# Kernel tuning notes

Measured on AMD Instinct MI355X. Metric: run time of the kernel, lower is better.

The kernel has to match this reference:

```python
import jax, jax.numpy as jnp
import numpy as np

BATCH, SEQ, DIMS, HEADS = 4, 2048, 1024, 16
HEAD_DIM = DIMS // HEADS          # 64
ROT = HEAD_DIM // 2               # 32
BASE = 10000.0


def setup_inputs() -> dict:
    key = jax.random.key(0)
    k1, k2, k3, k4 = jax.random.split(key, 4)
    x = jax.random.normal(k1, (BATCH, SEQ, DIMS), jnp.float32)
    thetas = jax.random.normal(k2, (ROT,), jnp.float32) * 0.02
    theta_scale = jnp.ones((1,), jnp.float32)
    # nn.init.orthogonal_ equivalent
    a = jax.random.normal(k3, (HEAD_DIM, HEAD_DIM), jnp.float32)
    r_matrix, _ = jnp.linalg.qr(a)
    inv_freq = 1.0 / (BASE ** (jnp.arange(0, HEAD_DIM, 2, dtype=jnp.float32) / HEAD_DIM))
    # r_pairs: torch rand(rot,2)*head_dim then .long() -> ints in [0, head_dim)
    pairs = jax.random.randint(k4, (ROT, 2), 0, HEAD_DIM, dtype=jnp.int32)
    return {"x": x, "thetas": thetas, "theta_scale": theta_scale,
            "r_matrix": r_matrix, "inv_freq": inv_freq, "pairs": pairs}


def _forward(x, thetas, theta_scale, r_matrix, inv_freq, pairs):
    B, S, D = x.shape
    hd = r_matrix.shape[0]
    H = D // hd
    ts = theta_scale[0]
    xf = x.reshape(-1, hd)  # (B*S*H, hd)

    # Sequential Givens rotations: x @ G_k, applied as 2-column updates.
    # G[i,i]=c, G[j,j]=c, G[i,j]=-s, G[j,i]=s. If i==j, sequential torch
    def body(xx, k):
        i, j = pairs[k, 0], pairs[k, 1]
        th = thetas[k] * ts
        c, s = jnp.cos(th), jnp.sin(th)
        xi = xx[:, i]
        xj = xx[:, j]
        ni = xi * c + xj * s
        nj = jnp.where(i == j, xi * s, xj * c - xi * s)
        xx = xx.at[:, i].set(ni)
        xx = xx.at[:, j].set(nj)  # overwrites column i when i == j
        return xx, None

    xf, _ = jax.lax.scan(body, xf, jnp.arange(pairs.shape[0]))
    xf = xf @ r_matrix
    xh = xf.reshape(B, S, H, hd)

    # rotary sin/cos encoding (concatenated halves, not interleaved)
    pos = jnp.arange(S, dtype=x.dtype)[:, None]          # (S, 1)
    si = pos * inv_freq[None, :]                          # (S, hd//2)
    sin = jnp.sin(si)[None, :, None, :]                   # (1, S, 1, hd//2)
    cos = jnp.cos(si)[None, :, None, :]
    x1, x2 = xh[..., ::2], xh[..., 1::2]
    out = jnp.concatenate([x1 * cos - x2 * sin, x1 * sin + x2 * cos], axis=-1)
    return out.reshape(B, S, D) * jnp.sqrt(jnp.asarray(D, x.dtype))


def reference(x, thetas, theta_scale, r_matrix, inv_freq, pairs):
    return _forward(x, thetas, theta_scale, r_matrix, inv_freq, pairs)
```

## Files before the change

kernel.cpp:

```cpp
#include <hip/hip_runtime.h>
#include <math.h>

#define SEQ    2048
#define ROT    32
#define NTILES 2048

__global__ __launch_bounds__(256) void build_w_kernel(
    const float* __restrict__ thetas,
    const float* __restrict__ theta_scale,
    const float* __restrict__ R,
    const int*   __restrict__ pairs,
    float*       __restrict__ Wp)
{
    __shared__ float A[64 * 65];
    const int t = threadIdx.x;

    #pragma unroll
    for (int i = 0; i < 16; ++i) {
        int e = i * 256 + t;
        int r = e >> 6, c = e & 63;
        A[r * 65 + c] = (r == c) ? 1.0f : 0.0f;
    }
    __syncthreads();

    if (t < 64) {
        const float ts = theta_scale[0];
        float* Ar = &A[t * 65];
        for (int k = 0; k < ROT; ++k) {
            int i = pairs[2 * k], j = pairs[2 * k + 1];
            float th = thetas[k] * ts;
            float c = cosf(th), s = sinf(th);
            float ai = Ar[i], aj = Ar[j];
            if (i != j) { Ar[i] = c * ai + s * aj; Ar[j] = c * aj - s * ai; }
            else        { Ar[i] = s * ai; }
        }
    }
    __syncthreads();

    const int r = (blockIdx.x << 2) + (t >> 6);
    const int c = t & 63;
    const float* Ar = &A[r * 65];
    float acc = 0.0f;
    #pragma unroll 8
    for (int k = 0; k < 64; ++k)
        acc = fmaf(Ar[k], R[k * 64 + c], acc);
    const int dest = (c & 1) ? (32 + (c >> 1)) : (c >> 1);
    Wp[r * 64 + dest] = 32.0f * acc;
}

__global__ __launch_bounds__(256) void rotary_main_kernel(
    const float* __restrict__ x,
    const float* __restrict__ Wp,
    const float* __restrict__ inv_freq,
    float*       __restrict__ out)
{
    __shared__ float  Xs[64 * 65];
    __shared__ float  Ws[64 * 64];
    __shared__ float2 SC[4 * 32];

    const int T    = blockIdx.x;
    const int t    = threadIdx.x;
    const int lane = t & 63;

    const float4* xg = (const float4*)(x + (size_t)T * 4096);
    #pragma unroll
    for (int i = 0; i < 4; ++i) {
        int g = i * 256 + t;
        float4 v = xg[g];
        int row = g >> 4;
        int col = (g & 15) << 2;
        float* p = &Xs[row * 65 + col];
        p[0] = v.x; p[1] = v.y; p[2] = v.z; p[3] = v.w;
    }
    {
        const float4* wg  = (const float4*)Wp;
        float4*       ws4 = (float4*)Ws;
        #pragma unroll
        for (int i = 0; i < 4; ++i) {
            int g = i * 256 + t;
            ws4[g] = wg[g];
        }
    }
    if (t < 128) {
        int pp = t >> 5, d = t & 31;
        int pos = (T * 4 + pp) & (SEQ - 1);
        float ang = (float)pos * inv_freq[d];
        float sv, cv;
        sincosf(ang, &sv, &cv);
        SC[t] = make_float2(cv, sv);
    }
    __syncthreads();

    const int cq = __builtin_amdgcn_readfirstlane(t >> 6);
    const float* xr = &Xs[lane * 65];
    const float* wc = &Ws[cq * 16];

    float acc[16];
    #pragma unroll
    for (int m = 0; m < 16; ++m) acc[m] = 0.0f;

    #pragma unroll 8
    for (int k = 0; k < 64; ++k) {
        float xv = xr[k];
        const float4 w0 = *(const float4*)(wc + k * 64);
        const float4 w1 = *(const float4*)(wc + k * 64 + 4);
        const float4 w2 = *(const float4*)(wc + k * 64 + 8);
        const float4 w3 = *(const float4*)(wc + k * 64 + 12);
        acc[ 0] = fmaf(xv, w0.x, acc[ 0]);
        acc[ 1] = fmaf(xv, w0.y, acc[ 1]);
        acc[ 2] = fmaf(xv, w0.z, acc[ 2]);
        acc[ 3] = fmaf(xv, w0.w, acc[ 3]);
        acc[ 4] = fmaf(xv, w1.x, acc[ 4]);
        acc[ 5] = fmaf(xv, w1.y, acc[ 5]);
        acc[ 6] = fmaf(xv, w1.z, acc[ 6]);
        acc[ 7] = fmaf(xv, w1.w, acc[ 7]);
        acc[ 8] = fmaf(xv, w2.x, acc[ 8]);
        acc[ 9] = fmaf(xv, w2.y, acc[ 9]);
        acc[10] = fmaf(xv, w2.z, acc[10]);
        acc[11] = fmaf(xv, w2.w, acc[11]);
        acc[12] = fmaf(xv, w3.x, acc[12]);
        acc[13] = fmaf(xv, w3.y, acc[13]);
        acc[14] = fmaf(xv, w3.z, acc[14]);
        acc[15] = fmaf(xv, w3.w, acc[15]);
    }

    __syncthreads();
    #pragma unroll
    for (int m = 0; m < 16; ++m)
        Xs[lane * 65 + cq * 16 + m] = acc[m];
    __syncthreads();

    float* og = out + (size_t)T * 4096;
    const int w = t >> 6;
    #pragma unroll
    for (int u = 0; u < 16; ++u) {
        int row = u * 4 + w;
        int d   = lane & 31;
        float yd = Xs[row * 65 + d];
        float y2 = Xs[row * 65 + 32 + d];
        float2 cs = SC[(row >> 4) * 32 + d];
        float o = (lane < 32) ? (yd * cs.x - y2 * cs.y)
                              : (yd * cs.y + y2 * cs.x);
        og[u * 256 + t] = o;
    }
}

extern "C" void kernel_launch(void* const* d_in, const int* in_sizes, int n_in,
                              void* d_out, int out_size, void* d_ws, size_t ws_size,
                              hipStream_t stream) {
    const float* x           = (const float*)d_in[0];
    const float* thetas      = (const float*)d_in[1];
    const float* theta_scale = (const float*)d_in[2];
    const float* r_matrix    = (const float*)d_in[3];
    const float* inv_freq    = (const float*)d_in[4];
    const int*   pairs       = (const int*)d_in[5];
    float*       out         = (float*)d_out;
    float*       Wp          = (float*)d_ws;

    build_w_kernel<<<16, 256, 0, stream>>>(thetas, theta_scale, r_matrix, pairs, Wp);
    rotary_main_kernel<<<NTILES, 256, 0, stream>>>(x, Wp, inv_freq, out);
}
```

Measured before the change: 119.1 us.

## Use 4x8 register tiles with XOR-swizzled transposed X tile and direct epilogue

Each block now handles 128 rows instead of 64. Each thread computes a 4x8 output tile from a transposed, XOR-swizzled shared-memory copy of X, so both operands are read as float4 and each loaded value is reused more times. The W column permutation is dropped: the rotary epilogue pairs adjacent accumulator columns in registers and writes float4 results straight to global memory, which removes the second shared-memory round trip and its barriers. Shared memory per block grows, which may lower occupancy, and the transposing stores into shared memory are scalar and scattered.

```diff
diff --git a/kernel.cpp b/kernel.cpp
--- a/kernel.cpp
+++ b/kernel.cpp
@@ -3,14 +3,15 @@
 
 #define SEQ    2048
 #define ROT    32
-#define NTILES 2048
+#define ROWS_PER_BLOCK 128
+#define NTILES (131072 / ROWS_PER_BLOCK)
 
 __global__ __launch_bounds__(256) void build_w_kernel(
     const float* __restrict__ thetas,
     const float* __restrict__ theta_scale,
     const float* __restrict__ R,
     const int*   __restrict__ pairs,
-    float*       __restrict__ Wp)
+    float*       __restrict__ W)
 {
     __shared__ float A[64 * 65];
     const int t = threadIdx.x;
@@ -44,104 +45,97 @@
     #pragma unroll 8
     for (int k = 0; k < 64; ++k)
         acc = fmaf(Ar[k], R[k * 64 + c], acc);
-    const int dest = (c & 1) ? (32 + (c >> 1)) : (c >> 1);
-    Wp[r * 64 + dest] = 32.0f * acc;
+    W[r * 64 + c] = 32.0f * acc;
 }
 
 __global__ __launch_bounds__(256) void rotary_main_kernel(
     const float* __restrict__ x,
-    const float* __restrict__ Wp,
+    const float* __restrict__ W,
     const float* __restrict__ inv_freq,
     float*       __restrict__ out)
 {
-    __shared__ float  Xs[64 * 65];
-    __shared__ float  Ws[64 * 64];
-    __shared__ float2 SC[4 * 32];
+    __shared__ float Xt[64 * 128];
+    __shared__ float Ws[64 * 64];
+    __shared__ float SCc[8 * 32];
+    __shared__ float SCs[8 * 32];
 
-    const int T    = blockIdx.x;
-    const int t    = threadIdx.x;
-    const int lane = t & 63;
+    const int T = blockIdx.x;
+    const int t = threadIdx.x;
 
-    const float4* xg = (const float4*)(x + (size_t)T * 4096);
+    const float4* xg = (const float4*)(x + (size_t)T * (ROWS_PER_BLOCK * 64));
     #pragma unroll
-    for (int i = 0; i < 4; ++i) {
-        int g = i * 256 + t;
+    for (int it = 0; it < 8; ++it) {
+        int g = it * 256 + t;
         float4 v = xg[g];
         int row = g >> 4;
-        int col = (g & 15) << 2;
-        float* p = &Xs[row * 65 + col];
-        p[0] = v.x; p[1] = v.y; p[2] = v.z; p[3] = v.w;
+        int k4  = (g & 15) << 2;
+        float vv[4] = {v.x, v.y, v.z, v.w};
+        #pragma unroll
+        for (int j = 0; j < 4; ++j) {
+            int k = k4 + j;
+            Xt[k * 128 + (((row >> 2) ^ (k & 31)) << 2) + (row & 3)] = vv[j];
+        }
     }
     {
-        const float4* wg  = (const float4*)Wp;
+        const float4* wg  = (const float4*)W;
         float4*       ws4 = (float4*)Ws;
         #pragma unroll
-        for (int i = 0; i < 4; ++i) {
-            int g = i * 256 + t;
-            ws4[g] = wg[g];
-        }
+        for (int i = 0; i < 4; ++i)
+            ws4[i * 256 + t] = wg[i * 256 + t];
     }
-    if (t < 128) {
-        int pp = t >> 5, d = t & 31;
-        int pos = (T * 4 + pp) & (SEQ - 1);
-        float ang = (float)pos * inv_freq[d];
+    {
+        int pg = t >> 5, d = t & 31;
+        int pos = (T * 8 + pg) & (SEQ - 1);
         float sv, cv;
-        sincosf(ang, &sv, &cv);
-        SC[t] = make_float2(cv, sv);
+        sincosf((float)pos * inv_freq[d], &sv, &cv);
+        SCc[t] = cv;
+        SCs[t] = sv;
     }
     __syncthreads();
 
-    const int cq = __builtin_amdgcn_readfirstlane(t >> 6);
-    const float* xr = &Xs[lane * 65];
-    const float* wc = &Ws[cq * 16];
+    const int rg = t >> 3;
+    const int cg = t & 7;
 
-    float acc[16];
+    float acc[4][8];
     #pragma unroll
-    for (int m = 0; m < 16; ++m) acc[m] = 0.0f;
+    for (int m = 0; m < 4; ++m)
+        #pragma unroll
+        for (int j = 0; j < 8; ++j) acc[m][j] = 0.0f;
 
-    #pragma unroll 8
+    #pragma unroll 4
     for (int k = 0; k < 64; ++k) {
-        float xv = xr[k];
-        const float4 w0 = *(const float4*)(wc + k * 64);
-        const float4 w1 = *(const float4*)(wc + k * 64 + 4);
-        const float4 w2 = *(const float4*)(wc + k * 64 + 8);
-        const float4 w3 = *(const float4*)(wc + k * 64 + 12);
-        acc[ 0] = fmaf(xv, w0.x, acc[ 0]);
-        acc[ 1] = fmaf(xv, w0.y, acc[ 1]);
-        acc[ 2] = fmaf(xv, w0.z, acc[ 2]);
-        acc[ 3] = fmaf(xv, w0.w, acc[ 3]);
-        acc[ 4] = fmaf(xv, w1.x, acc[ 4]);
-        acc[ 5] = fmaf(xv, w1.y, acc[ 5]);
-        acc[ 6] = fmaf(xv, w1.z, acc[ 6]);
-        acc[ 7] = fmaf(xv, w1.w, acc[ 7]);
-        acc[ 8] = fmaf(xv, w2.x, acc[ 8]);
-        acc[ 9] = fmaf(xv, w2.y, acc[ 9]);
-        acc[10] = fmaf(xv, w2.z, acc[10]);
-        acc[11] = fmaf(xv, w2.w, acc[11]);
-        acc[12] = fmaf(xv, w3.x, acc[12]);
-        acc[13] = fmaf(xv, w3.y, acc[13]);
-        acc[14] = fmaf(xv, w3.z, acc[14]);
-        acc[15] = fmaf(xv, w3.w, acc[15]);
+        const float4 xv = *(const float4*)&Xt[k * 128 + ((rg ^ (k & 31)) << 2)];
+        const float4 w0 = *(const float4*)&Ws[k * 64 + cg * 8];
+        const float4 w1 = *(const float4*)&Ws[k * 64 + cg * 8 + 4];
+        const float xs[4] = {xv.x, xv.y, xv.z, xv.w};
+        const float ws[8] = {w0.x, w0.y, w0.z, w0.w, w1.x, w1.y, w1.z, w1.w};
+        #pragma unroll
+        for (int m = 0; m < 4; ++m)
+            #pragma unroll
+            for (int j = 0; j < 8; ++j)
+                acc[m][j] = fmaf(xs[m], ws[j], acc[m][j]);
     }
 
-    __syncthreads();
+    const int scb = (rg >> 2) * 32 + cg * 4;
+    const float4 cv = *(const float4*)&SCc[scb];
+    const float4 sv = *(const float4*)&SCs[scb];
+    const float cs4[4] = {cv.x, cv.y, cv.z, cv.w};
+    const float sn4[4] = {sv.x, sv.y, sv.z, sv.w};
+
+    float* og = out + (size_t)T * (ROWS_PER_BLOCK * 64);
     #pragma unroll
-    for (int m = 0; m < 16; ++m)
-        Xs[lane * 65 + cq * 16 + m] = acc[m];
-    __syncthreads();
-
-    float* og = out + (size_t)T * 4096;
-    const int w = t >> 6;
-    #pragma unroll
-    for (int u = 0; u < 16; ++u) {
-        int row = u * 4 + w;
-        int d   = lane & 31;
-        float yd = Xs[row * 65 + d];
-        float y2 = Xs[row * 65 + 32 + d];
-        float2 cs = SC[(row >> 4) * 32 + d];
-        float o = (lane < 32) ? (yd * cs.x - y2 * cs.y)
-                              : (yd * cs.y + y2 * cs.x);
-        og[u * 256 + t] = o;
+    for (int m = 0; m < 4; ++m) {
+        int row = rg * 4 + m;
+        float o1[4], o2[4];
+        #pragma unroll
+        for (int d = 0; d < 4; ++d) {
+            float a = acc[m][2 * d];
+            float b = acc[m][2 * d + 1];
+            o1[d] = a * cs4[d] - b * sn4[d];
+            o2[d] = a * sn4[d] + b * cs4[d];
+        }
+        *(float4*)&og[row * 64 + cg * 4]      = make_float4(o1[0], o1[1], o1[2], o1[3]);
+        *(float4*)&og[row * 64 + 32 + cg * 4] = make_float4(o2[0], o2[1], o2[2], o2[3]);
     }
 }
 
@@ -155,8 +149,8 @@
     const float* inv_freq    = (const float*)d_in[4];
     const int*   pairs       = (const int*)d_in[5];
     float*       out         = (float*)d_out;
-    float*       Wp          = (float*)d_ws;
+    float*       W           = (float*)d_ws;
 
-    build_w_kernel<<<16, 256, 0, stream>>>(thetas, theta_scale, r_matrix, pairs, Wp);
-    rotary_main_kernel<<<NTILES, 256, 0, stream>>>(x, Wp, inv_freq, out);
+    build_w_kernel<<<16, 256, 0, stream>>>(thetas, theta_scale, r_matrix, pairs, W);
+    rotary_main_kernel<<<NTILES, 256, 0, stream>>>(x, W, inv_freq, out);
 }
```

After: 112.7 us. -5.4%, faster.
